# Optimization experiments

Hardware: AMD Instinct MI355X
Metric: run time of the kernel (lower is better)

Reference implementation:

```python
import jax, jax.numpy as jnp
import numpy as np

B, S, H, A = 2, 1024, 512, 128


def setup_inputs() -> dict:
    key = jax.random.key(0)
    k1, k2, k3, k4 = jax.random.split(key, 4)
    lstm_output = jax.random.normal(k1, (B, S, H), dtype=jnp.float32)
    w = jax.random.normal(k2, (H, A), dtype=jnp.float32) / np.sqrt(H)
    u = jax.random.normal(k3, (H, A), dtype=jnp.float32) / np.sqrt(H)
    v = jax.random.normal(k4, (A,), dtype=jnp.float32) / np.sqrt(A)
    return {"lstm_output": lstm_output, "w": w, "u": u, "v": v}


def reference(lstm_output, w, u, v):
    # lstm_output: (B,S,H); w,u: (H,A); v: (A,)
    wx = jnp.einsum('bsh,ha->bsa', lstm_output, w)   # (B,S,A)
    ux = jnp.einsum('bsh,ha->bsa', lstm_output, u)   # (B,S,A)
    # e[b,i,j] = tanh(wx[b,i] + ux[b,j]) . v  -> (B,S,S), via (B,S,S,A) intermediate
    e = jnp.einsum('bija,a->bij', jnp.tanh(wx[:, :, None, :] + ux[:, None, :, :]), v)
    attention_weights = jax.nn.softmax(e, axis=-1)   # (B,S,S)
    # bmm(attn, lstm_output) -> (B,S,H), then sum over dim 1 -> (B,H)
    context_vector = jnp.einsum('bij,bjh->bh', attention_weights, lstm_output)
    return context_vector, attention_weights
```

## Files before the change

### kernel.cpp

```cpp
#include <hip/hip_runtime.h>

#define HH   512
#define AA   128
#define SB   1024
#define BATCH 2

__device__ __forceinline__ float fast_rcp(float x) { return __builtin_amdgcn_rcpf(x); }
__device__ __forceinline__ float fast_ex2(float x) { return __builtin_amdgcn_exp2f(x); }

__global__ __launch_bounds__(256) void k1_gemm(const float* __restrict__ lstm,
                                               const float* __restrict__ w,
                                               const float* __restrict__ u,
                                               float* __restrict__ part0,
                                               float* __restrict__ part1,
                                               float* __restrict__ colw)
{
    __shared__ float As[32][68];
    __shared__ float Bs[32][36];
    const int t  = threadIdx.x;
    const int bx = blockIdx.x, by = blockIdx.y, bz = blockIdx.z;
    const int m0 = bx * 64;
    const int n0 = by * 32;
    const float* __restrict__ Bsrc = (n0 < AA) ? w : u;
    const int ncol = n0 & (AA - 1);

    if (bx == 0 && by == 0) {
        float4 z4; z4.x = z4.y = z4.z = z4.w = 0.f;
        ((float4*)colw)[bz * 256 + t] = z4;
    }

    const int r  = t & 63;
    const int kq = (t >> 6) * 8;
    const int kk = t >> 3;
    const int nq = (t & 7) * 4;
    const int tm = t >> 4;
    const int tn = t & 15;

    float acc[4][2];
    #pragma unroll
    for (int i = 0; i < 4; ++i) { acc[i][0] = 0.f; acc[i][1] = 0.f; }

    for (int kc = 0; kc < 8; ++kc) {
        const int k0 = bz * 256 + kc * 32;
        const float* ap = &lstm[(size_t)(m0 + r) * HH + k0 + kq];
        const float4 a0 = *(const float4*)&ap[0];
        const float4 a1 = *(const float4*)&ap[4];
        As[kq + 0][r] = a0.x; As[kq + 1][r] = a0.y;
        As[kq + 2][r] = a0.z; As[kq + 3][r] = a0.w;
        As[kq + 4][r] = a1.x; As[kq + 5][r] = a1.y;
        As[kq + 6][r] = a1.z; As[kq + 7][r] = a1.w;
        const float4 bv = *(const float4*)&Bsrc[(size_t)(k0 + kk) * AA + ncol + nq];
        *(float4*)&Bs[kk][nq] = bv;
        __syncthreads();
        #pragma unroll
        for (int k = 0; k < 32; ++k) {
            const float4 av = *(const float4*)&As[k][4 * tm];
            const float2 bb = *(const float2*)&Bs[k][2 * tn];
            acc[0][0] = fmaf(av.x, bb.x, acc[0][0]);
            acc[0][1] = fmaf(av.x, bb.y, acc[0][1]);
            acc[1][0] = fmaf(av.y, bb.x, acc[1][0]);
            acc[1][1] = fmaf(av.y, bb.y, acc[1][1]);
            acc[2][0] = fmaf(av.z, bb.x, acc[2][0]);
            acc[2][1] = fmaf(av.z, bb.y, acc[2][1]);
            acc[3][0] = fmaf(av.w, bb.x, acc[3][0]);
            acc[3][1] = fmaf(av.w, bb.y, acc[3][1]);
        }
        __syncthreads();
    }

    float* __restrict__ part = bz ? part1 : part0;
    #pragma unroll
    for (int mi = 0; mi < 4; ++mi) {
        float2 st; st.x = acc[mi][0]; st.y = acc[mi][1];
        *(float2*)&part[(size_t)(m0 + 4 * tm + mi) * 256 + n0 + 2 * tn] = st;
    }
}

__global__ __launch_bounds__(256) void k1b_combine_exp(const float* __restrict__ part0,
                                                       const float* __restrict__ part1,
                                                       float* __restrict__ P,
                                                       float* __restrict__ Q)
{
    const float KK = 2.8853900817779268f;
    const int idx = blockIdx.x * 256 + threadIdx.x;
    const float4 c0 = ((const float4*)part0)[idx];
    const float4 c1 = ((const float4*)part1)[idx];
    float4 o;
    o.x = fast_ex2(KK * (c0.x + c1.x));
    o.y = fast_ex2(KK * (c0.y + c1.y));
    o.z = fast_ex2(KK * (c0.z + c1.z));
    o.w = fast_ex2(KK * (c0.w + c1.w));
    const int m  = idx >> 6;
    const int qd = idx & 63;
    float* dst = (qd < 32) ? &P[(size_t)m * AA + qd * 4]
                           : &Q[(size_t)m * AA + (qd - 32) * 4];
    *(float4*)dst = o;
}

__global__ __launch_bounds__(1024) void k2_fused(const float* __restrict__ P,
                                                 const float* __restrict__ Q,
                                                 const float* __restrict__ v,
                                                 float* __restrict__ attn,
                                                 float* __restrict__ colw,
                                                 float* __restrict__ ctx)
{
    const int b  = blockIdx.y;
    const int i0 = blockIdx.x * 8;
    const int j  = threadIdx.x;

    if (blockIdx.x == 0 && j < HH) ctx[b * HH + j] = 0.f;

    const float* __restrict__ Qrow = &Q[((size_t)b * SB + j) * AA];
    const float* __restrict__ Pb   = &P[((size_t)b * SB + i0) * AA];

    float acc[8];
    #pragma unroll
    for (int i = 0; i < 8; ++i) acc[i] = 0.f;
    float Vacc = 0.f;

    #pragma unroll 2
    for (int x = 0; x < 32; ++x) {
        const float4 q4 = *(const float4*)&Qrow[x * 4];
        const float4 vv = *(const float4*)&v[x * 4];
        Vacc += (vv.x + vv.y) + (vv.z + vv.w);
        #pragma unroll
        for (int i = 0; i < 8; ++i) {
            const float4 p = *(const float4*)&Pb[i * AA + x * 4];
            const float d0 = fmaf(p.x, q4.x, 1.0f);
            const float d1 = fmaf(p.y, q4.y, 1.0f);
            const float d2 = fmaf(p.z, q4.z, 1.0f);
            const float d3 = fmaf(p.w, q4.w, 1.0f);
            const float na = fmaf(vv.y, d0, vv.x * d1);
            const float nb = fmaf(vv.w, d2, vv.z * d3);
            const float ra = fast_rcp(d0 * d1);
            const float rb = fast_rcp(d2 * d3);
            acc[i] = fmaf(na, ra, acc[i]);
            acc[i] = fmaf(nb, rb, acc[i]);
        }
    }

    const float L2E  = 1.4426950408889634f;
    const float base = Vacc * L2E;
    float E[8];
    #pragma unroll
    for (int i = 0; i < 8; ++i)
        E[i] = fast_ex2(fmaf(acc[i], -2.0f * L2E, base));

    __shared__ float red[8][16];
    const int lane = j & 63, wv = j >> 6;
    #pragma unroll
    for (int i = 0; i < 8; ++i) {
        float s = E[i];
        #pragma unroll
        for (int off = 32; off > 0; off >>= 1) s += __shfl_xor(s, off);
        if (lane == 0) red[i][wv] = s;
    }
    __syncthreads();

    float csum = 0.f;
    float* __restrict__ arow = &attn[((size_t)b * SB + i0) * SB + j];
    #pragma unroll
    for (int i = 0; i < 8; ++i) {
        const float4* rr = (const float4*)red[i];
        const float4 r0 = rr[0], r1 = rr[1], r2 = rr[2], r3 = rr[3];
        const float rs = ((r0.x + r0.y) + (r0.z + r0.w)) + ((r1.x + r1.y) + (r1.z + r1.w))
                       + ((r2.x + r2.y) + (r2.z + r2.w)) + ((r3.x + r3.y) + (r3.z + r3.w));
        const float a = E[i] * fast_rcp(rs);
        arow[(size_t)i * SB] = a;
        csum += a;
    }
    atomicAdd(&colw[b * SB + j], csum);
}

__global__ __launch_bounds__(256) void k4_context(const float* __restrict__ lstm,
                                                  const float* __restrict__ colw,
                                                  float* __restrict__ ctx)
{
    const int b  = blockIdx.z;
    const int h  = blockIdx.x * 256 + threadIdx.x;
    const int j0 = blockIdx.y * 128;
    __shared__ float cw[128];
    if (threadIdx.x < 128) cw[threadIdx.x] = colw[b * SB + j0 + threadIdx.x];
    __syncthreads();
    float acc = 0.f;
    #pragma unroll 8
    for (int jj = 0; jj < 128; ++jj)
        acc = fmaf(cw[jj], lstm[(size_t)(b * SB + j0 + jj) * HH + h], acc);
    atomicAdd(&ctx[b * HH + h], acc);
}

extern "C" void kernel_launch(void* const* d_in, const int* in_sizes, int n_in,
                              void* d_out, int out_size, void* d_ws, size_t ws_size,
                              hipStream_t stream)
{
    const float* lstm = (const float*)d_in[0];
    const float* w    = (const float*)d_in[1];
    const float* u    = (const float*)d_in[2];
    const float* v    = (const float*)d_in[3];

    float* out  = (float*)d_out;
    float* ctx  = out;
    float* attn = out + BATCH * HH;

    float* part0 = (float*)d_ws;
    float* part1 = part0 + (size_t)2048 * 256;
    float* P     = part1 + (size_t)2048 * 256;
    float* Qb    = P     + (size_t)BATCH * SB * AA;
    float* colw  = Qb    + (size_t)BATCH * SB * AA;

    k1_gemm<<<dim3(32, 8, 2), 256, 0, stream>>>(lstm, w, u, part0, part1, colw);
    k1b_combine_exp<<<dim3(512), 256, 0, stream>>>(part0, part1, P, Qb);
    k2_fused<<<dim3(128, BATCH), 1024, 0, stream>>>(P, Qb, v, attn, colw, ctx);
    k4_context<<<dim3(2, 8, BATCH), 256, 0, stream>>>(lstm, colw, ctx);
}
```

Measured before the change: 62.95 us.

## Split fused score kernel, retile GEMM to 4x4, and make column sums atomic-free

The GEMM now uses 64x64 tiles with a 4x4 register micro-tile and a 4-way split-K, so the combine kernel sums four partials. The fused score/softmax kernel is split in two. The first kernel uses 256-thread blocks, prefetches Q registers, folds the per-quad reciprocals into one, writes unnormalized exponentials and atomically accumulates row sums. The second kernel rescales attention in place and writes per-block column partials that the context kernel reduces, replacing the colw atomics. This is meant to raise occupancy and cut transcendental work in the hot loop, at the cost of an extra launch and an extra read/write pass over the 8 MB attention matrix.

```diff
diff --git a/kernel.cpp b/kernel.cpp
--- a/kernel.cpp
+++ b/kernel.cpp
@@ -8,88 +8,99 @@
 __device__ __forceinline__ float fast_rcp(float x) { return __builtin_amdgcn_rcpf(x); }
 __device__ __forceinline__ float fast_ex2(float x) { return __builtin_amdgcn_exp2f(x); }
 
+__device__ __forceinline__ void quad_acc(const float4 p, const float4 q4,
+                                         const float4 vv, float& acc)
+{
+    const float d0 = fmaf(p.x, q4.x, 1.0f);
+    const float d1 = fmaf(p.y, q4.y, 1.0f);
+    const float d2 = fmaf(p.z, q4.z, 1.0f);
+    const float d3 = fmaf(p.w, q4.w, 1.0f);
+    const float p01 = d0 * d1, p23 = d2 * d3;
+    const float na = fmaf(vv.x, d1, vv.y * d0);
+    const float nb = fmaf(vv.z, d3, vv.w * d2);
+    const float N  = fmaf(na, p23, nb * p01);
+    acc = fmaf(N, fast_rcp(p01 * p23), acc);
+}
+
 __global__ __launch_bounds__(256) void k1_gemm(const float* __restrict__ lstm,
                                                const float* __restrict__ w,
                                                const float* __restrict__ u,
-                                               float* __restrict__ part0,
-                                               float* __restrict__ part1,
-                                               float* __restrict__ colw)
-{
-    __shared__ float As[32][68];
-    __shared__ float Bs[32][36];
+                                               float* __restrict__ parts,
+                                               float* __restrict__ rsum,
+                                               float* __restrict__ ctx)
+{
+    __shared__ float As[16][68];
+    __shared__ float Bs[16][68];
     const int t  = threadIdx.x;
     const int bx = blockIdx.x, by = blockIdx.y, bz = blockIdx.z;
     const int m0 = bx * 64;
-    const int n0 = by * 32;
+    const int n0 = by * 64;
     const float* __restrict__ Bsrc = (n0 < AA) ? w : u;
-    const int ncol = n0 & (AA - 1);
-
-    if (bx == 0 && by == 0) {
-        float4 z4; z4.x = z4.y = z4.z = z4.w = 0.f;
-        ((float4*)colw)[bz * 256 + t] = z4;
-    }
-
-    const int r  = t & 63;
-    const int kq = (t >> 6) * 8;
-    const int kk = t >> 3;
-    const int nq = (t & 7) * 4;
-    const int tm = t >> 4;
-    const int tn = t & 15;
-
-    float acc[4][2];
-    #pragma unroll
-    for (int i = 0; i < 4; ++i) { acc[i][0] = 0.f; acc[i][1] = 0.f; }
-
+    const int nc = n0 & (AA - 1);
+
+    if (bx == 0) {
+        if (by == 0)      { rsum[bz * 512 + t] = 0.f; rsum[bz * 512 + 256 + t] = 0.f; }
+        else if (by == 1) { ctx[bz * 256 + t] = 0.f; }
+    }
+
+    const int ar = t >> 2, aq = (t & 3) * 4;
+    const int bk = t >> 4, bq = (t & 15) * 4;
+    const int tm = (t >> 4) * 4, tn = (t & 15) * 4;
+
+    float acc[4][4];
+    #pragma unroll
+    for (int mi = 0; mi < 4; ++mi)
+        #pragma unroll
+        for (int ni = 0; ni < 4; ++ni) acc[mi][ni] = 0.f;
+
+    const int kz0 = bz * 128;
     for (int kc = 0; kc < 8; ++kc) {
-        const int k0 = bz * 256 + kc * 32;
-        const float* ap = &lstm[(size_t)(m0 + r) * HH + k0 + kq];
-        const float4 a0 = *(const float4*)&ap[0];
-        const float4 a1 = *(const float4*)&ap[4];
-        As[kq + 0][r] = a0.x; As[kq + 1][r] = a0.y;
-        As[kq + 2][r] = a0.z; As[kq + 3][r] = a0.w;
-        As[kq + 4][r] = a1.x; As[kq + 5][r] = a1.y;
-        As[kq + 6][r] = a1.z; As[kq + 7][r] = a1.w;
-        const float4 bv = *(const float4*)&Bsrc[(size_t)(k0 + kk) * AA + ncol + nq];
-        *(float4*)&Bs[kk][nq] = bv;
+        const int k0 = kz0 + kc * 16;
+        const float4 a4 = *(const float4*)&lstm[(size_t)(m0 + ar) * HH + k0 + aq];
+        const float4 b4 = *(const float4*)&Bsrc[(size_t)(k0 + bk) * AA + nc + bq];
+        As[aq + 0][ar] = a4.x; As[aq + 1][ar] = a4.y;
+        As[aq + 2][ar] = a4.z; As[aq + 3][ar] = a4.w;
+        *(float4*)&Bs[bk][bq] = b4;
         __syncthreads();
         #pragma unroll
-        for (int k = 0; k < 32; ++k) {
-            const float4 av = *(const float4*)&As[k][4 * tm];
-            const float2 bb = *(const float2*)&Bs[k][2 * tn];
-            acc[0][0] = fmaf(av.x, bb.x, acc[0][0]);
-            acc[0][1] = fmaf(av.x, bb.y, acc[0][1]);
-            acc[1][0] = fmaf(av.y, bb.x, acc[1][0]);
-            acc[1][1] = fmaf(av.y, bb.y, acc[1][1]);
-            acc[2][0] = fmaf(av.z, bb.x, acc[2][0]);
-            acc[2][1] = fmaf(av.z, bb.y, acc[2][1]);
-            acc[3][0] = fmaf(av.w, bb.x, acc[3][0]);
-            acc[3][1] = fmaf(av.w, bb.y, acc[3][1]);
+        for (int k = 0; k < 16; ++k) {
+            const float4 av = *(const float4*)&As[k][tm];
+            const float4 bv = *(const float4*)&Bs[k][tn];
+            #pragma unroll
+            for (int mi = 0; mi < 4; ++mi) {
+                const float a = (mi == 0) ? av.x : (mi == 1) ? av.y : (mi == 2) ? av.z : av.w;
+                acc[mi][0] = fmaf(a, bv.x, acc[mi][0]);
+                acc[mi][1] = fmaf(a, bv.y, acc[mi][1]);
+                acc[mi][2] = fmaf(a, bv.z, acc[mi][2]);
+                acc[mi][3] = fmaf(a, bv.w, acc[mi][3]);
+            }
         }
         __syncthreads();
     }
 
-    float* __restrict__ part = bz ? part1 : part0;
+    float* __restrict__ part = parts + (size_t)bz * (2048 * 256);
     #pragma unroll
     for (int mi = 0; mi < 4; ++mi) {
-        float2 st; st.x = acc[mi][0]; st.y = acc[mi][1];
-        *(float2*)&part[(size_t)(m0 + 4 * tm + mi) * 256 + n0 + 2 * tn] = st;
-    }
-}
-
-__global__ __launch_bounds__(256) void k1b_combine_exp(const float* __restrict__ part0,
-                                                       const float* __restrict__ part1,
+        float4 s; s.x = acc[mi][0]; s.y = acc[mi][1]; s.z = acc[mi][2]; s.w = acc[mi][3];
+        *(float4*)&part[(size_t)(m0 + tm + mi) * 256 + n0 + tn] = s;
+    }
+}
+
+__global__ __launch_bounds__(256) void k1b_combine_exp(const float* __restrict__ parts,
                                                        float* __restrict__ P,
                                                        float* __restrict__ Q)
 {
     const float KK = 2.8853900817779268f;
     const int idx = blockIdx.x * 256 + threadIdx.x;
-    const float4 c0 = ((const float4*)part0)[idx];
-    const float4 c1 = ((const float4*)part1)[idx];
+    const float4 c0 = ((const float4*)parts)[idx];
+    const float4 c1 = ((const float4*)parts)[idx + 131072];
+    const float4 c2 = ((const float4*)parts)[idx + 262144];
+    const float4 c3 = ((const float4*)parts)[idx + 393216];
     float4 o;
-    o.x = fast_ex2(KK * (c0.x + c1.x));
-    o.y = fast_ex2(KK * (c0.y + c1.y));
-    o.z = fast_ex2(KK * (c0.z + c1.z));
-    o.w = fast_ex2(KK * (c0.w + c1.w));
+    o.x = fast_ex2(KK * ((c0.x + c1.x) + (c2.x + c3.x)));
+    o.y = fast_ex2(KK * ((c0.y + c1.y) + (c2.y + c3.y)));
+    o.z = fast_ex2(KK * ((c0.z + c1.z) + (c2.z + c3.z)));
+    o.w = fast_ex2(KK * ((c0.w + c1.w) + (c2.w + c3.w)));
     const int m  = idx >> 6;
     const int qd = idx & 63;
     float* dst = (qd < 32) ? &P[(size_t)m * AA + qd * 4]
@@ -97,95 +108,112 @@
     *(float4*)dst = o;
 }
 
-__global__ __launch_bounds__(1024) void k2_fused(const float* __restrict__ P,
-                                                 const float* __restrict__ Q,
-                                                 const float* __restrict__ v,
-                                                 float* __restrict__ attn,
-                                                 float* __restrict__ colw,
-                                                 float* __restrict__ ctx)
+__global__ __launch_bounds__(256) void k2a_escore(const float* __restrict__ P,
+                                                  const float* __restrict__ Q,
+                                                  const float* __restrict__ v,
+                                                  float* __restrict__ E,
+                                                  float* __restrict__ rsum)
+{
+    const int b  = blockIdx.z;
+    const int i0 = blockIdx.y * 8;
+    const int j  = blockIdx.x * 256 + threadIdx.x;
+
+    const float4* __restrict__ Qr = (const float4*)&Q[((size_t)b * SB + j) * AA];
+    const float*  __restrict__ Pb = &P[((size_t)b * SB + i0) * AA];
+
+    float acc[8];
+    #pragma unroll
+    for (int i = 0; i < 8; ++i) acc[i] = 0.f;
+    float Vacc = 0.f;
+
+    float4 qc[4], qn[4];
+    #pragma unroll
+    for (int x2 = 0; x2 < 4; ++x2) qc[x2] = Qr[x2];
+
+    for (int xc = 0; xc < 8; ++xc) {
+        const int nb4 = (xc < 7) ? (xc + 1) * 4 : 0;
+        #pragma unroll
+        for (int x2 = 0; x2 < 4; ++x2) qn[x2] = Qr[nb4 + x2];
+        #pragma unroll
+        for (int x2 = 0; x2 < 4; ++x2) {
+            const float4 q4 = qc[x2];
+            const float4 vv = *(const float4*)&v[(xc * 4 + x2) * 4];
+            Vacc += (vv.x + vv.y) + (vv.z + vv.w);
+            #pragma unroll
+            for (int i = 0; i < 8; ++i) {
+                const float4 p = *(const float4*)&Pb[(size_t)i * AA + (xc * 4 + x2) * 4];
+                quad_acc(p, q4, vv, acc[i]);
+            }
+        }
+        #pragma unroll
+        for (int x2 = 0; x2 < 4; ++x2) qc[x2] = qn[x2];
+    }
+
+    const float L2E  = 1.4426950408889634f;
+    const float base = Vacc * L2E;
+    float* __restrict__ Eout = &E[((size_t)(b * SB + i0)) * SB + j];
+    const int lane = threadIdx.x & 63;
+    #pragma unroll
+    for (int i = 0; i < 8; ++i) {
+        const float e = fast_ex2(fmaf(acc[i], -2.0f * L2E, base));
+        Eout[(size_t)i * SB] = e;
+        float s = e;
+        #pragma unroll
+        for (int off = 32; off > 0; off >>= 1) s += __shfl_xor(s, off);
+        if (lane == 0) atomicAdd(&rsum[b * SB + i0 + i], s);
+    }
+}
+
+__global__ __launch_bounds__(1024) void k2b_scale_colpart(float* __restrict__ attn,
+                                                          const float* __restrict__ rsum,
+                                                          float* __restrict__ colw_part)
 {
     const int b  = blockIdx.y;
     const int i0 = blockIdx.x * 8;
     const int j  = threadIdx.x;
 
-    if (blockIdx.x == 0 && j < HH) ctx[b * HH + j] = 0.f;
-
-    const float* __restrict__ Qrow = &Q[((size_t)b * SB + j) * AA];
-    const float* __restrict__ Pb   = &P[((size_t)b * SB + i0) * AA];
-
-    float acc[8];
-    #pragma unroll
-    for (int i = 0; i < 8; ++i) acc[i] = 0.f;
-    float Vacc = 0.f;
-
-    #pragma unroll 2
-    for (int x = 0; x < 32; ++x) {
-        const float4 q4 = *(const float4*)&Qrow[x * 4];
-        const float4 vv = *(const float4*)&v[x * 4];
-        Vacc += (vv.x + vv.y) + (vv.z + vv.w);
-        #pragma unroll
-        for (int i = 0; i < 8; ++i) {
-            const float4 p = *(const float4*)&Pb[i * AA + x * 4];
-            const float d0 = fmaf(p.x, q4.x, 1.0f);
-            const float d1 = fmaf(p.y, q4.y, 1.0f);
-            const float d2 = fmaf(p.z, q4.z, 1.0f);
-            const float d3 = fmaf(p.w, q4.w, 1.0f);
-            const float na = fmaf(vv.y, d0, vv.x * d1);
-            const float nb = fmaf(vv.w, d2, vv.z * d3);
-            const float ra = fast_rcp(d0 * d1);
-            const float rb = fast_rcp(d2 * d3);
-            acc[i] = fmaf(na, ra, acc[i]);
-            acc[i] = fmaf(nb, rb, acc[i]);
-        }
-    }
-
-    const float L2E  = 1.4426950408889634f;
-    const float base = Vacc * L2E;
-    float E[8];
-    #pragma unroll
-    for (int i = 0; i < 8; ++i)
-        E[i] = fast_ex2(fmaf(acc[i], -2.0f * L2E, base));
-
-    __shared__ float red[8][16];
-    const int lane = j & 63, wv = j >> 6;
+    float csum = 0.f;
     #pragma unroll
     for (int i = 0; i < 8; ++i) {
-        float s = E[i];
-        #pragma unroll
-        for (int off = 32; off > 0; off >>= 1) s += __shfl_xor(s, off);
-        if (lane == 0) red[i][wv] = s;
-    }
+        const int row = b * SB + i0 + i;
+        const float inv = fast_rcp(rsum[row]);
+        float* __restrict__ ap = &attn[(size_t)row * SB + j];
+        const float a = (*ap) * inv;
+        *ap = a;
+        csum += a;
+    }
+    colw_part[((size_t)b * 128 + blockIdx.x) * SB + j] = csum;
+}
+
+__global__ __launch_bounds__(256) void k4_context(const float* __restrict__ lstm,
+                                                  const float* __restrict__ colw_part,
+                                                  float* __restrict__ ctx)
+{
+    const int b  = blockIdx.z;
+    const int j0 = blockIdx.y * 32;
+    const int h  = blockIdx.x * 256 + threadIdx.x;
+
+    __shared__ float red[8][33];
+    __shared__ float cw[32];
+    const int jj = threadIdx.x & 31, grp = threadIdx.x >> 5;
+    float s = 0.f;
+    #pragma unroll
+    for (int k2 = 0; k2 < 16; ++k2)
+        s += colw_part[((size_t)b * 128 + grp * 16 + k2) * SB + j0 + jj];
+    red[grp][jj] = s;
     __syncthreads();
-
-    float csum = 0.f;
-    float* __restrict__ arow = &attn[((size_t)b * SB + i0) * SB + j];
-    #pragma unroll
-    for (int i = 0; i < 8; ++i) {
-        const float4* rr = (const float4*)red[i];
-        const float4 r0 = rr[0], r1 = rr[1], r2 = rr[2], r3 = rr[3];
-        const float rs = ((r0.x + r0.y) + (r0.z + r0.w)) + ((r1.x + r1.y) + (r1.z + r1.w))
-                       + ((r2.x + r2.y) + (r2.z + r2.w)) + ((r3.x + r3.y) + (r3.z + r3.w));
-        const float a = E[i] * fast_rcp(rs);
-        arow[(size_t)i * SB] = a;
-        csum += a;
-    }
-    atomicAdd(&colw[b * SB + j], csum);
-}
-
-__global__ __launch_bounds__(256) void k4_context(const float* __restrict__ lstm,
-                                                  const float* __restrict__ colw,
-                                                  float* __restrict__ ctx)
-{
-    const int b  = blockIdx.z;
-    const int h  = blockIdx.x * 256 + threadIdx.x;
-    const int j0 = blockIdx.y * 128;
-    __shared__ float cw[128];
-    if (threadIdx.x < 128) cw[threadIdx.x] = colw[b * SB + j0 + threadIdx.x];
+    if (threadIdx.x < 32) {
+        float c = 0.f;
+        #pragma unroll
+        for (int g = 0; g < 8; ++g) c += red[g][threadIdx.x];
+        cw[threadIdx.x] = c;
+    }
     __syncthreads();
+
     float acc = 0.f;
-    #pragma unroll 8
-    for (int jj = 0; jj < 128; ++jj)
-        acc = fmaf(cw[jj], lstm[(size_t)(b * SB + j0 + jj) * HH + h], acc);
+    #pragma unroll
+    for (int x = 0; x < 32; ++x)
+        acc = fmaf(cw[x], lstm[(size_t)(b * SB + j0 + x) * HH + h], acc);
     atomicAdd(&ctx[b * HH + h], acc);
 }
 
@@ -202,14 +230,15 @@
     float* ctx  = out;
     float* attn = out + BATCH * HH;
 
-    float* part0 = (float*)d_ws;
-    float* part1 = part0 + (size_t)2048 * 256;
-    float* P     = part1 + (size_t)2048 * 256;
-    float* Qb    = P     + (size_t)BATCH * SB * AA;
-    float* colw  = Qb    + (size_t)BATCH * SB * AA;
-
-    k1_gemm<<<dim3(32, 8, 2), 256, 0, stream>>>(lstm, w, u, part0, part1, colw);
-    k1b_combine_exp<<<dim3(512), 256, 0, stream>>>(part0, part1, P, Qb);
-    k2_fused<<<dim3(128, BATCH), 1024, 0, stream>>>(P, Qb, v, attn, colw, ctx);
-    k4_context<<<dim3(2, 8, BATCH), 256, 0, stream>>>(lstm, colw, ctx);
-}
+    float* parts     = (float*)d_ws;
+    float* P         = parts + (size_t)4 * 2048 * 256;
+    float* Qb        = P     + (size_t)BATCH * SB * AA;
+    float* rsum      = Qb    + (size_t)BATCH * SB * AA;
+    float* colw_part = rsum  + (size_t)BATCH * SB;
+
+    k1_gemm<<<dim3(32, 4, 4), 256, 0, stream>>>(lstm, w, u, parts, rsum, ctx);
+    k1b_combine_exp<<<dim3(512), 256, 0, stream>>>(parts, P, Qb);
+    k2a_escore<<<dim3(4, 128, BATCH), 256, 0, stream>>>(P, Qb, v, attn, rsum);
+    k2b_scale_colpart<<<dim3(128, BATCH), 1024, 0, stream>>>(attn, rsum, colw_part);
+    k4_context<<<dim3(2, 32, BATCH), 256, 0, stream>>>(lstm, colw_part, ctx);
+}
```

Result: slower. 73.72 us (+17.1%).
